# Kernel optimization log

Measured on AMD Instinct MI355X. Metric: run time of the kernel, lower is better.

## Reference

```python
import jax, jax.numpy as jnp
import numpy as np
from jax import lax

B, T, I, H = 32, 512, 512, 1024


def setup_inputs() -> dict:
    key = jax.random.key(0)
    k0, k1, k2, k3, k4 = jax.random.split(key, 5)
    s_i = 1.0 / np.sqrt(I).astype(np.float32)
    s_h = 1.0 / np.sqrt(H).astype(np.float32)
    x = jax.random.normal(k0, (B, T, I), dtype=jnp.float32)
    # stacked gate weights, order: input(i), forget(f), cell(g), output(o)
    Wx = jax.random.uniform(k1, (4 * H, I), jnp.float32, -s_i, s_i)
    bx = jax.random.uniform(k2, (4 * H,), jnp.float32, -s_i, s_i)
    Wh = jax.random.uniform(k3, (4 * H, H), jnp.float32, -s_h, s_h)
    bh = jax.random.uniform(k4, (4 * H,), jnp.float32, -s_h, s_h)
    return {"x": x, "Wx": Wx, "bx": bx, "Wh": Wh, "bh": bh}


def reference(x, Wx, bx, Wh, bh):
    # Pre-compute all input-to-gate projections in one batched GEMM: [B,T,4H]
    xg = jnp.einsum("bti,gi->btg", x, Wx) + bx + bh

    def step(carry, xg_t):
        h, c = carry
        gates = xg_t + h @ Wh.T  # [B,4H]
        i, f, g, o = jnp.split(gates, 4, axis=-1)
        i = jax.nn.sigmoid(i)
        f = jax.nn.sigmoid(f)
        g = jnp.tanh(g)
        o = jax.nn.sigmoid(o)
        c = f * c + i * g
        h = o * jnp.tanh(c)  # r is None in forward -> h_tilde = tanh(c)
        return (h, c), h

    b = x.shape[0]
    h0 = jnp.zeros((b, H), dtype=x.dtype)
    c0 = jnp.zeros((b, H), dtype=x.dtype)
    _, hs = lax.scan(step, (h0, c0), jnp.swapaxes(xg, 0, 1))  # hs: [T,B,H]
    return jnp.swapaxes(hs, 0, 1)  # [B,T,H]
```

## Files before the change

### kernel.cpp

```cpp
#include <hip/hip_runtime.h>
#include <hip/hip_bf16.h>

#define Bv 32
#define Tv 512
#define Iv 512
#define Hv 1024
#define NG 4096

typedef short bf16x8 __attribute__((ext_vector_type(8)));
typedef float floatx16 __attribute__((ext_vector_type(16)));
typedef unsigned short u16;
typedef unsigned long long u64;

__device__ __forceinline__ u16 f2bf(float f) {
  __hip_bfloat16 h = __float2bfloat16(f);
  return *reinterpret_cast<u16*>(&h);
}

__device__ __forceinline__ floatx16 mfma32(bf16x8 a, bf16x8 b, floatx16 c) {
  return __builtin_amdgcn_mfma_f32_32x32x16_bf16(a, b, c, 0, 0, 0);
}

__device__ __forceinline__ u64 ld_agent_u64(const u64* p) {
  return __hip_atomic_load(p, __ATOMIC_RELAXED, __HIP_MEMORY_SCOPE_AGENT);
}
__device__ __forceinline__ void st_agent_u16(u16* p, u16 v) {
  __hip_atomic_store(p, v, __ATOMIC_RELAXED, __HIP_MEMORY_SCOPE_AGENT);
}

__device__ __forceinline__ bf16x8 mk_frag(u64 lo, u64 hi) {
  union { u64 q[2]; bf16x8 v; } u;
  u.q[0] = lo; u.q[1] = hi;
  return u.v;
}

__global__ void k_init(unsigned int* p, int n) {
  int i = blockIdx.x * blockDim.x + threadIdx.x;
  if (i < n) p[i] = 0u;
}

__global__ void k_f2bf(const float* __restrict__ in, u16* __restrict__ out, int n) {
  int i = blockIdx.x * blockDim.x + threadIdx.x;
  if (i < n) out[i] = f2bf(in[i]);
}

__global__ void k_whf(const float* __restrict__ Wh, u16* __restrict__ whf) {
  int tid = blockIdx.x * 256 + threadIdx.x;
  int lane = tid & 63;
  int kt   = (tid >> 6) & 63;
  int nt   = (tid >> 12) & 1;
  int bl   = tid >> 13;
  int r    = nt * 32 + (lane & 31);
  int gate = r >> 4, du = r & 15;
  int row  = gate * Hv + bl * 16 + du;
  int k0   = kt * 16 + (lane >> 5) * 8;
  const float* s = Wh + (size_t)row * Hv + k0;
  u16* d = whf + (size_t)tid * 8;
#pragma unroll
  for (int j = 0; j < 8; ++j) d[j] = f2bf(s[j]);
}

__global__ __launch_bounds__(256) void k_xg(const u16* __restrict__ xb, const u16* __restrict__ wxb,
                                            const float* __restrict__ bx, const float* __restrict__ bh,
                                            float* __restrict__ xg, int t0, int tcshift) {
  __shared__ u16 Al[128 * 40];
  __shared__ u16 Bl[128 * 40];
  int tid = threadIdx.x;
  int wave = tid >> 6, lane = tid & 63;
  int wm = wave & 1, wn = wave >> 1;
  int bm = blockIdx.x, bn = blockIdx.y;
  int Tc = 1 << tcshift;

  floatx16 acc[2][2];
#pragma unroll
  for (int a = 0; a < 2; ++a)
#pragma unroll
    for (int c = 0; c < 2; ++c)
#pragma unroll
      for (int r = 0; r < 16; ++r) acc[a][c][r] = 0.f;

  int lr = tid >> 1;
  int lk = (tid & 1) * 16;
  int m  = bm * 128 + lr;
  int b  = m >> tcshift;
  int tl = m & (Tc - 1);
  const u16* asrc = xb + (size_t)(b * Tv + t0 + tl) * Iv + lk;
  int nrow = bn * 128 + lr;
  const u16* bsrc = wxb + (size_t)nrow * Iv + lk;
  u16* adst = &Al[lr * 40 + lk];
  u16* bdst = &Bl[lr * 40 + lk];

  for (int k0 = 0; k0 < Iv; k0 += 32) {
    __syncthreads();
    *(uint4*)adst       = *(const uint4*)(asrc);
    *(uint4*)(adst + 8) = *(const uint4*)(asrc + 8);
    *(uint4*)bdst       = *(const uint4*)(bsrc);
    *(uint4*)(bdst + 8) = *(const uint4*)(bsrc + 8);
    asrc += 32; bsrc += 32;
    __syncthreads();
#pragma unroll
    for (int kt = 0; kt < 2; ++kt) {
      int ko = kt * 16 + (lane >> 5) * 8;
      bf16x8 a0 = *(const bf16x8*)(&Al[(wm * 64 +      (lane & 31)) * 40 + ko]);
      bf16x8 a1 = *(const bf16x8*)(&Al[(wm * 64 + 32 + (lane & 31)) * 40 + ko]);
      bf16x8 b0 = *(const bf16x8*)(&Bl[(wn * 64 +      (lane & 31)) * 40 + ko]);
      bf16x8 b1 = *(const bf16x8*)(&Bl[(wn * 64 + 32 + (lane & 31)) * 40 + ko]);
      acc[0][0] = mfma32(a0, b0, acc[0][0]);
      acc[0][1] = mfma32(a0, b1, acc[0][1]);
      acc[1][0] = mfma32(a1, b0, acc[1][0]);
      acc[1][1] = mfma32(a1, b1, acc[1][1]);
    }
  }
#pragma unroll
  for (int mt = 0; mt < 2; ++mt) {
#pragma unroll
    for (int ntt = 0; ntt < 2; ++ntt) {
      int nGl = bn * 128 + wn * 64 + ntt * 32 + (lane & 31);
      float bias = bx[nGl] + bh[nGl];
#pragma unroll
      for (int r = 0; r < 16; ++r) {
        int mrow = (r & 3) + 8 * (r >> 2) + 4 * (lane >> 5);
        int mG = bm * 128 + wm * 64 + mt * 32 + mrow;
        int bb = mG >> tcshift;
        int tt = mG & (Tc - 1);
        xg[((size_t)(tt * Bv + bb) << 12) + nGl] = acc[mt][ntt][r] + bias;
      }
    }
  }
}

__global__ __launch_bounds__(256, 1) void k_scan(const u16* __restrict__ whf, const float* __restrict__ xg,
                                                 u64* __restrict__ hA, float* __restrict__ cbuf,
                                                 float* __restrict__ out, int* cnt, int t0, int Tc) {
  __shared__ float red[4][64][36];
  int tid = threadIdx.x;
  int bl = blockIdx.x;
  int kh = tid >> 6, lane = tid & 63;
  int eu = tid & 15, eb = tid >> 4;
  int u0 = bl * 16;

  bf16x8 w0[16], w1[16];
  {
    const u16* wb0 = whf + ((size_t)(bl * 2 + 0) << 15);
    const u16* wb1 = whf + ((size_t)(bl * 2 + 1) << 15);
#pragma unroll
    for (int kk = 0; kk < 16; ++kk) {
      int kt = kh * 16 + kk;
      w0[kk] = *(const bf16x8*)(wb0 + (size_t)((kt << 6) + lane) * 8);
      w1[kk] = *(const bf16x8*)(wb1 + (size_t)((kt << 6) + lane) * 8);
    }
  }

  float c0, c1;
  if (t0 == 0) { c0 = 0.f; c1 = 0.f; }
  else {
    c0 = cbuf[eb * Hv + u0 + eu];
    c1 = cbuf[(eb + 16) * Hv + u0 + eu];
  }

  u16* hA16 = (u16*)hA;

  float xgv[4][2];
#pragma unroll
  for (int g = 0; g < 4; ++g)
#pragma unroll
    for (int b2 = 0; b2 < 2; ++b2)
      xgv[g][b2] = xg[((size_t)(0 * Bv + eb + 16 * b2) << 12) + g * Hv + u0 + eu];

  for (int tl = 0; tl < Tc; ++tl) {
    int t = t0 + tl;
    const u64* hAr = hA + (size_t)(t & 1) * 8192;

    floatx16 acc0, acc1;
#pragma unroll
    for (int r = 0; r < 16; ++r) { acc0[r] = 0.f; acc1[r] = 0.f; }
#pragma unroll
    for (int kk = 0; kk < 16; ++kk) {
      int kt = kh * 16 + kk;
      size_t fi = (size_t)((kt << 6) + lane) * 2;
      bf16x8 a = mk_frag(ld_agent_u64(hAr + fi), ld_agent_u64(hAr + fi + 1));
      acc0 = mfma32(a, w0[kk], acc0);
      acc1 = mfma32(a, w1[kk], acc1);
    }

    {
      int n = lane & 31;
      int bq = 4 * (lane >> 5);
#pragma unroll
      for (int rq = 0; rq < 4; ++rq) {
        float4 v0 = make_float4(acc0[rq * 4 + 0], acc0[rq * 4 + 1], acc0[rq * 4 + 2], acc0[rq * 4 + 3]);
        float4 v1 = make_float4(acc1[rq * 4 + 0], acc1[rq * 4 + 1], acc1[rq * 4 + 2], acc1[rq * 4 + 3]);
        *(float4*)&red[kh][n][8 * rq + bq]      = v0;
        *(float4*)&red[kh][32 + n][8 * rq + bq] = v1;
      }
    }

    float xgn[4][2];
    {
      int tln = (tl + 1 < Tc) ? tl + 1 : tl;
#pragma unroll
      for (int g = 0; g < 4; ++g)
#pragma unroll
        for (int b2 = 0; b2 < 2; ++b2)
          xgn[g][b2] = xg[((size_t)(tln * Bv + eb + 16 * b2) << 12) + g * Hv + u0 + eu];
    }

    __syncthreads();

    u16* hAw16 = hA16 + (size_t)((t + 1) & 1) * 32768;
#pragma unroll
    for (int b2 = 0; b2 < 2; ++b2) {
      int b = eb + 16 * b2;
      float gsum[4];
#pragma unroll
      for (int g = 0; g < 4; ++g) {
        int r = g * 16 + eu;
        gsum[g] = red[0][r][b] + red[1][r][b] + red[2][r][b] + red[3][r][b] + xgv[g][b2];
      }
      float iv = 1.f / (1.f + __expf(-gsum[0]));
      float fv = 1.f / (1.f + __expf(-gsum[1]));
      float gv = 1.f - 2.f / (__expf(2.f * gsum[2]) + 1.f);
      float ov = 1.f / (1.f + __expf(-gsum[3]));
      float& c = b2 ? c1 : c0;
      c = fv * c + iv * gv;
      float hval = ov * (1.f - 2.f / (__expf(2.f * c) + 1.f));
      st_agent_u16(hAw16 + ((size_t)((bl << 6) + b + ((eu >> 3) << 5)) << 3) + (eu & 7), f2bf(hval));
      out[((size_t)(b * Tv + t) << 10) + u0 + eu] = hval;
    }

    asm volatile("s_waitcnt vmcnt(0)" ::: "memory");
    __syncthreads();
    if (tid == 0) {
      __hip_atomic_fetch_add(cnt, 1, __ATOMIC_RELAXED, __HIP_MEMORY_SCOPE_AGENT);
      int target = 64 * (t + 1);
      while (__hip_atomic_load(cnt, __ATOMIC_RELAXED, __HIP_MEMORY_SCOPE_AGENT) < target) { }
    }
    __syncthreads();

#pragma unroll
    for (int g = 0; g < 4; ++g)
#pragma unroll
      for (int b2 = 0; b2 < 2; ++b2) xgv[g][b2] = xgn[g][b2];
  }
  cbuf[eb * Hv + u0 + eu] = c0;
  cbuf[(eb + 16) * Hv + u0 + eu] = c1;
}

extern "C" void kernel_launch(void* const* d_in, const int* in_sizes, int n_in,
                              void* d_out, int out_size, void* d_ws, size_t ws_size,
                              hipStream_t stream) {
  const float* x  = (const float*)d_in[0];
  const float* Wx = (const float*)d_in[1];
  const float* bx = (const float*)d_in[2];
  const float* Wh = (const float*)d_in[3];
  const float* bh = (const float*)d_in[4];
  float* out = (float*)d_out;
  char* ws = (char*)d_ws;

  int*   cnt = (int*)ws;
  u64*   hA  = (u64*)(ws + 4096);
  float* cb  = (float*)(ws + 4096 + (128 << 10));
  u16*   xb  = (u16*)(ws + 4096 + (256 << 10));
  u16*   wxb = xb + (size_t)Bv * Tv * Iv;
  u16*   whf = wxb + (size_t)NG * Iv;
  float* xg  = (float*)(whf + (size_t)64 * 2 * 64 * 64 * 8);

  size_t fixedB = 4096 + (256ull << 10) +
                  ((size_t)Bv * Tv * Iv + (size_t)NG * Iv + (size_t)64 * 2 * 64 * 64 * 8) * 2;
  int tcshift = 9;
  while (tcshift > 2 && fixedB + (((size_t)Bv * NG * 4) << tcshift) > ws_size) --tcshift;
  int Tc = 1 << tcshift;

  k_init<<<132, 256, 0, stream>>>((unsigned int*)ws, (4096 + (128 << 10)) / 4);
  k_f2bf<<<(Bv * Tv * Iv) / 256, 256, 0, stream>>>(x, xb, Bv * Tv * Iv);
  k_f2bf<<<(NG * Iv) / 256, 256, 0, stream>>>(Wx, wxb, NG * Iv);
  k_whf<<<2048, 256, 0, stream>>>(Wh, whf);

  for (int t0 = 0; t0 < Tv; t0 += Tc) {
    k_xg<<<dim3(Tc / 4, 32), 256, 0, stream>>>(xb, wxb, bx, bh, xg, t0, tcshift);
    k_scan<<<64, 256, 0, stream>>>(whf, xg, hA, cb, out, cnt, t0, Tc);
  }
}
```

Before: 2.688 ms.

## Replace global counter barrier with per-wave producer flags in LSTM scan

Replaces the per-step grid-wide atomic counter barrier with per-wave flags. Each wave publishes its own completion flag, and each lane polls only the producer flag covering the hidden-state slice its wave needs. The reduction buffer is double-buffered by timestep parity, which removes the trailing __syncthreads. Hidden-state loads are batched ahead of the MFMAs, and the output and next-step xg loads are moved after the flag publish. This shortens the serial critical path per step. The risk is that a fast block may overwrite the ping-pong h buffer before a block it does not depend on has finished reading it.

New measurement: 3.043 ms. 1.13x slower.

```diff
diff --git a/kernel.cpp b/kernel.cpp
--- a/kernel.cpp
+++ b/kernel.cpp
@@ -131,8 +131,8 @@
 
 __global__ __launch_bounds__(256, 1) void k_scan(const u16* __restrict__ whf, const float* __restrict__ xg,
                                                  u64* __restrict__ hA, float* __restrict__ cbuf,
-                                                 float* __restrict__ out, int* cnt, int t0, int Tc) {
-  __shared__ float red[4][64][36];
+                                                 float* __restrict__ out, int* flags, int t0, int Tc) {
+  __shared__ float red[2][4][64][36];
   int tid = threadIdx.x;
   int bl = blockIdx.x;
   int kh = tid >> 6, lane = tid & 63;
@@ -159,6 +159,7 @@
   }
 
   u16* hA16 = (u16*)hA;
+  int* fp = flags + (kh << 6) + lane;
 
   float xgv[4][2];
 #pragma unroll
@@ -169,16 +170,28 @@
 
   for (int tl = 0; tl < Tc; ++tl) {
     int t = t0 + tl;
+
+    while (__hip_atomic_load(fp, __ATOMIC_RELAXED, __HIP_MEMORY_SCOPE_AGENT) < t) {
+      __builtin_amdgcn_s_sleep(0);
+    }
+    asm volatile("" ::: "memory");
+
     const u64* hAr = hA + (size_t)(t & 1) * 8192;
 
+    u64 alo[16], ahi[16];
+#pragma unroll
+    for (int kk = 0; kk < 16; ++kk) {
+      size_t fi = (size_t)((((kh << 4) + kk) << 6) + lane) * 2;
+      alo[kk] = ld_agent_u64(hAr + fi);
+      ahi[kk] = ld_agent_u64(hAr + fi + 1);
+    }
+
     floatx16 acc0, acc1;
 #pragma unroll
     for (int r = 0; r < 16; ++r) { acc0[r] = 0.f; acc1[r] = 0.f; }
 #pragma unroll
     for (int kk = 0; kk < 16; ++kk) {
-      int kt = kh * 16 + kk;
-      size_t fi = (size_t)((kt << 6) + lane) * 2;
-      bf16x8 a = mk_frag(ld_agent_u64(hAr + fi), ld_agent_u64(hAr + fi + 1));
+      bf16x8 a = mk_frag(alo[kk], ahi[kk]);
       acc0 = mfma32(a, w0[kk], acc0);
       acc1 = mfma32(a, w1[kk], acc1);
     }
@@ -190,57 +203,59 @@
       for (int rq = 0; rq < 4; ++rq) {
         float4 v0 = make_float4(acc0[rq * 4 + 0], acc0[rq * 4 + 1], acc0[rq * 4 + 2], acc0[rq * 4 + 3]);
         float4 v1 = make_float4(acc1[rq * 4 + 0], acc1[rq * 4 + 1], acc1[rq * 4 + 2], acc1[rq * 4 + 3]);
-        *(float4*)&red[kh][n][8 * rq + bq]      = v0;
-        *(float4*)&red[kh][32 + n][8 * rq + bq] = v1;
+        *(float4*)&red[t & 1][kh][n][8 * rq + bq]      = v0;
+        *(float4*)&red[t & 1][kh][32 + n][8 * rq + bq] = v1;
       }
     }
 
-    float xgn[4][2];
+    __syncthreads();
+
+    float hv0, hv1;
+    {
+      float gs[4][2];
+#pragma unroll
+      for (int g = 0; g < 4; ++g) {
+        int r = g * 16 + eu;
+#pragma unroll
+        for (int b2 = 0; b2 < 2; ++b2) {
+          int b = eb + 16 * b2;
+          gs[g][b2] = red[t & 1][0][r][b] + red[t & 1][1][r][b] +
+                      red[t & 1][2][r][b] + red[t & 1][3][r][b] + xgv[g][b2];
+        }
+      }
+      float i0 = 1.f / (1.f + __expf(-gs[0][0]));
+      float f0 = 1.f / (1.f + __expf(-gs[1][0]));
+      float g0 = 1.f - 2.f / (__expf(2.f * gs[2][0]) + 1.f);
+      float o0 = 1.f / (1.f + __expf(-gs[3][0]));
+      c0 = f0 * c0 + i0 * g0;
+      hv0 = o0 * (1.f - 2.f / (__expf(2.f * c0) + 1.f));
+
+      float i1 = 1.f / (1.f + __expf(-gs[0][1]));
+      float f1 = 1.f / (1.f + __expf(-gs[1][1]));
+      float g1 = 1.f - 2.f / (__expf(2.f * gs[2][1]) + 1.f);
+      float o1 = 1.f / (1.f + __expf(-gs[3][1]));
+      c1 = f1 * c1 + i1 * g1;
+      hv1 = o1 * (1.f - 2.f / (__expf(2.f * c1) + 1.f));
+    }
+
+    u16* hAw16 = hA16 + (size_t)((t + 1) & 1) * 32768;
+    st_agent_u16(hAw16 + ((size_t)((bl << 6) + eb +      ((eu >> 3) << 5)) << 3) + (eu & 7), f2bf(hv0));
+    st_agent_u16(hAw16 + ((size_t)((bl << 6) + eb + 16 + ((eu >> 3) << 5)) << 3) + (eu & 7), f2bf(hv1));
+    asm volatile("s_waitcnt vmcnt(0)" ::: "memory");
+    if (lane == 0)
+      __hip_atomic_store(flags + (bl << 2) + kh, t + 1, __ATOMIC_RELAXED, __HIP_MEMORY_SCOPE_AGENT);
+
+    out[((size_t)(eb * Tv + t) << 10) + u0 + eu] = hv0;
+    out[((size_t)((eb + 16) * Tv + t) << 10) + u0 + eu] = hv1;
+
     {
       int tln = (tl + 1 < Tc) ? tl + 1 : tl;
 #pragma unroll
       for (int g = 0; g < 4; ++g)
 #pragma unroll
         for (int b2 = 0; b2 < 2; ++b2)
-          xgn[g][b2] = xg[((size_t)(tln * Bv + eb + 16 * b2) << 12) + g * Hv + u0 + eu];
-    }
-
-    __syncthreads();
-
-    u16* hAw16 = hA16 + (size_t)((t + 1) & 1) * 32768;
-#pragma unroll
-    for (int b2 = 0; b2 < 2; ++b2) {
-      int b = eb + 16 * b2;
-      float gsum[4];
-#pragma unroll
-      for (int g = 0; g < 4; ++g) {
-        int r = g * 16 + eu;
-        gsum[g] = red[0][r][b] + red[1][r][b] + red[2][r][b] + red[3][r][b] + xgv[g][b2];
-      }
-      float iv = 1.f / (1.f + __expf(-gsum[0]));
-      float fv = 1.f / (1.f + __expf(-gsum[1]));
-      float gv = 1.f - 2.f / (__expf(2.f * gsum[2]) + 1.f);
-      float ov = 1.f / (1.f + __expf(-gsum[3]));
-      float& c = b2 ? c1 : c0;
-      c = fv * c + iv * gv;
-      float hval = ov * (1.f - 2.f / (__expf(2.f * c) + 1.f));
-      st_agent_u16(hAw16 + ((size_t)((bl << 6) + b + ((eu >> 3) << 5)) << 3) + (eu & 7), f2bf(hval));
-      out[((size_t)(b * Tv + t) << 10) + u0 + eu] = hval;
-    }
-
-    asm volatile("s_waitcnt vmcnt(0)" ::: "memory");
-    __syncthreads();
-    if (tid == 0) {
-      __hip_atomic_fetch_add(cnt, 1, __ATOMIC_RELAXED, __HIP_MEMORY_SCOPE_AGENT);
-      int target = 64 * (t + 1);
-      while (__hip_atomic_load(cnt, __ATOMIC_RELAXED, __HIP_MEMORY_SCOPE_AGENT) < target) { }
-    }
-    __syncthreads();
-
-#pragma unroll
-    for (int g = 0; g < 4; ++g)
-#pragma unroll
-      for (int b2 = 0; b2 < 2; ++b2) xgv[g][b2] = xgn[g][b2];
+          xgv[g][b2] = xg[((size_t)(tln * Bv + eb + 16 * b2) << 12) + g * Hv + u0 + eu];
+    }
   }
   cbuf[eb * Hv + u0 + eu] = c0;
   cbuf[(eb + 16) * Hv + u0 + eu] = c1;
@@ -257,7 +272,7 @@
   float* out = (float*)d_out;
   char* ws = (char*)d_ws;
 
-  int*   cnt = (int*)ws;
+  int*   flags = (int*)ws;
   u64*   hA  = (u64*)(ws + 4096);
   float* cb  = (float*)(ws + 4096 + (128 << 10));
   u16*   xb  = (u16*)(ws + 4096 + (256 << 10));
@@ -278,6 +293,6 @@
 
   for (int t0 = 0; t0 < Tv; t0 += Tc) {
     k_xg<<<dim3(Tc / 4, 32), 256, 0, stream>>>(xb, wxb, bx, bh, xg, t0, tcshift);
-    k_scan<<<64, 256, 0, stream>>>(whf, xg, hA, cb, out, cnt, t0, Tc);
-  }
-}
+    k_scan<<<64, 256, 0, stream>>>(whf, xg, hA, cb, out, flags, t0, Tc);
+  }
+}
```
